# Performance work log

Measured on AMD Instinct MI355X. Metric: run time of the kernel, lower is better.

## Reference

```python
import jax, jax.numpy as jnp
import numpy as np

N_NODES = 10000
N_MOTIFS = 2500          # N_NODES / subgraph_size(=4)
N_AUG = N_NODES + N_MOTIFS
N_EDGES = 500000
NFEAT = 512
NHID = 128


def setup_inputs() -> dict:
    key = jax.random.key(0)
    ks = jax.random.split(key, 14)
    s = 0.05  # param init scale
    return {
        "x": jax.random.normal(ks[0], (N_NODES, NFEAT), jnp.float32),
        "edge_index": jax.random.randint(ks[1], (2, N_EDGES), 0, N_AUG, jnp.int64),
        "motif_list": jax.random.randint(ks[2], (N_MOTIFS, 4), 0, N_NODES, jnp.int64),
        "W1": jax.random.normal(ks[3], (NFEAT, 2 * NHID), jnp.float32) * s,
        "a_src1": jax.random.normal(ks[4], (2 * NHID,), jnp.float32) * s,
        "a_dst1": jax.random.normal(ks[5], (2 * NHID,), jnp.float32) * s,
        "b1": jnp.zeros((2 * NHID,), jnp.float32),
        "W2": jax.random.normal(ks[6], (2 * NHID, NHID), jnp.float32) * s,
        "a_src2": jax.random.normal(ks[7], (NHID,), jnp.float32) * s,
        "a_dst2": jax.random.normal(ks[8], (NHID,), jnp.float32) * s,
        "b2": jnp.zeros((NHID,), jnp.float32),
        "W_lin": jax.random.normal(ks[9], (NFEAT, NHID), jnp.float32) * s,  # torch Linear(nhid, nfeat) weight
        "b_lin": jnp.zeros((NFEAT,), jnp.float32),
    }


def gat_layer(x, src, dst, W, a_s, a_d, b, n):
    """Single-head GATConv (PyG semantics): edge-softmax attention over dst."""
    h = x @ W                                              # [n, out]
    alpha_s = h @ a_s                                      # [n]
    alpha_d = h @ a_d                                      # [n]
    e = jax.nn.leaky_relu(alpha_s[src] + alpha_d[dst], 0.2)  # [E]
    m = jax.ops.segment_max(e, dst, num_segments=n)        # stable softmax per dst
    w = jnp.exp(e - m[dst])
    denom = jax.ops.segment_sum(w, dst, num_segments=n)
    coef = w / (denom[dst] + 1e-16)                        # [E]
    out = jax.ops.segment_sum(coef[:, None] * h[src], dst, num_segments=n)
    return out + b


def reference(x, edge_index, motif_list, W1, a_src1, a_dst1, b1,
              W2, a_src2, a_dst2, b2, W_lin, b_lin):
    n = x.shape[0] + motif_list.shape[0]
    # augmented features: mean of each motif's node features appended as motif nodes
    x_aug = jnp.concatenate([x, jnp.mean(x[motif_list], axis=1)], axis=0)  # [N_AUG, F]
    # augmented edge list + self loops (GATConv adds self loops)
    loops = jnp.arange(n, dtype=edge_index.dtype)
    src = jnp.concatenate([edge_index[0], loops])
    dst = jnp.concatenate([edge_index[1], loops])
    h1 = gat_layer(x_aug, src, dst, W1, a_src1, a_dst1, b1, n)   # [N_AUG, 2*NHID]
    h2 = gat_layer(h1, src, dst, W2, a_src2, a_dst2, b2, n)      # [N_AUG, NHID]
    rec_adj = jax.nn.sigmoid(h2 @ h2.T)                          # [N_AUG, N_AUG]
    rec_feature = jax.nn.sigmoid(h2 @ W_lin.T + b_lin)           # [N_AUG, NFEAT]
    return (rec_feature, rec_adj)
```

## Files before the change

### kernel.cpp

```cpp
#include <hip/hip_runtime.h>

typedef unsigned short u16;
typedef unsigned int   u32;
typedef __attribute__((ext_vector_type(8))) short short8;
typedef __attribute__((ext_vector_type(4))) float f32x4;

#define N_NODES 10000
#define N_MOTIFS 2500
#define N_AUG   12500
#define N_EDGES 500000
#define E_TOT   512500
#define NFEAT   512
#define NH1     256
#define NH2     128

__device__ __forceinline__ float b2f(u16 u){ return __uint_as_float(((u32)u) << 16); }
__device__ __forceinline__ u16 f2b(float f){
  u32 x = __float_as_uint(f);
  x += 0x7fffu + ((x >> 16) & 1u);
  return (u16)(x >> 16);
}

#define PREP_Z   (N_AUG + 8)
#define PREP_W1  (NFEAT * NH1)
#define PREP_W2  (NH1 * NH2)
#define PREP_WL  (NFEAT * NH2)
#define PREP_B   (NH2)
#define PREP_TOT (PREP_Z + PREP_W1 + PREP_W2 + PREP_WL + PREP_B)

__global__ void k_prep(const float* __restrict__ W1, const float* __restrict__ W2,
                       const float* __restrict__ Wl, const float* __restrict__ b1,
                       int* __restrict__ cnt,
                       u16* __restrict__ W1T, u16* __restrict__ W2T, u16* __restrict__ Wlb,
                       float* __restrict__ b1W2){
  int i = blockIdx.x * blockDim.x + threadIdx.x;
  if (i < PREP_Z){ cnt[i] = 0; return; }
  i -= PREP_Z;
  if (i < PREP_W1){
    int r = i / NH1, c = i - r * NH1;
    W1T[(size_t)c * NFEAT + r] = f2b(W1[i]);
    return;
  }
  i -= PREP_W1;
  if (i < PREP_W2){
    int r = i / NH2, c = i - r * NH2;
    W2T[(size_t)c * NH1 + r] = f2b(W2[i]);
    return;
  }
  i -= PREP_W2;
  if (i < PREP_WL){ Wlb[i] = f2b(Wl[i]); return; }
  i -= PREP_WL;
  if (i < PREP_B){
    float s = 0.f;
    #pragma unroll 8
    for (int k = 0; k < NH1; ++k) s += b1[k] * W2[(size_t)k * NH2 + i];
    b1W2[i] = s;
  }
}

__global__ void k_xaug(const float* __restrict__ x, const int* __restrict__ motif,
                       u16* __restrict__ xb){
  int gid = blockIdx.x * blockDim.x + threadIdx.x;
  int row = gid >> 6;
  int c   = (gid & 63) << 3;
  if (row >= N_AUG) return;
  float v[8];
  if (row < N_NODES){
    const float* s = &x[(size_t)row * NFEAT + c];
    #pragma unroll
    for (int k = 0; k < 8; ++k) v[k] = s[k];
  } else {
    int m = row - N_NODES;
    const float* p0 = &x[(size_t)motif[m*4+0] * NFEAT + c];
    const float* p1 = &x[(size_t)motif[m*4+1] * NFEAT + c];
    const float* p2 = &x[(size_t)motif[m*4+2] * NFEAT + c];
    const float* p3 = &x[(size_t)motif[m*4+3] * NFEAT + c];
    #pragma unroll
    for (int k = 0; k < 8; ++k) v[k] = (p0[k] + p1[k] + p2[k] + p3[k]) * 0.25f;
  }
  short8 o;
  #pragma unroll
  for (int k = 0; k < 8; ++k) o[k] = (short)f2b(v[k]);
  *(short8*)&xb[(size_t)row * NFEAT + c] = o;
}

__global__ void k_hist(const int* __restrict__ ei, int* __restrict__ cnt){
  int i = blockIdx.x * blockDim.x + threadIdx.x;
  if (i >= E_TOT) return;
  int d = (i < N_EDGES) ? ei[N_EDGES + i] : (i - N_EDGES);
  atomicAdd(&cnt[d], 1);
}

__global__ void k_scan(const int* __restrict__ cnt, int* __restrict__ offs, int* __restrict__ cur){
  __shared__ int part[1024];
  int t = threadIdx.x;
  const int CH = 13;
  int base = t * CH;
  int s = 0;
  for (int i = 0; i < CH; ++i){ int idx = base + i; if (idx < N_AUG) s += cnt[idx]; }
  part[t] = s;
  __syncthreads();
  for (int off = 1; off < 1024; off <<= 1){
    int v = 0;
    if (t >= off) v = part[t - off];
    __syncthreads();
    if (t >= off) part[t] += v;
    __syncthreads();
  }
  int run = (t == 0) ? 0 : part[t - 1];
  for (int i = 0; i < CH; ++i){
    int idx = base + i;
    if (idx <= N_AUG){
      offs[idx] = run;
      if (idx < N_AUG){ cur[idx] = run; run += cnt[idx]; }
    }
  }
}

__global__ void k_scatter(const int* __restrict__ ei, int* __restrict__ cur, int* __restrict__ srcs){
  int i = blockIdx.x * blockDim.x + threadIdx.x;
  if (i >= E_TOT) return;
  int s, d;
  if (i < N_EDGES){ s = ei[i]; d = ei[N_EDGES + i]; } else { s = i - N_EDGES; d = s; }
  int pos = atomicAdd(&cur[d], 1);
  srcs[pos] = s;
}

template<int DIM>
__global__ void k_alpha(const u16* __restrict__ h, const float* __restrict__ avs,
                        const float* __restrict__ avd, float* __restrict__ oS, float* __restrict__ oD){
  __shared__ float shS[8], shD[8];
  int n = blockIdx.x, t = threadIdx.x;
  int lane = t & 63, wid = t >> 6;
  float hv = b2f(h[(size_t)n * DIM + t]);
  float s = hv * avs[t];
  float d = hv * avd[t];
  #pragma unroll
  for (int o = 32; o; o >>= 1){ s += __shfl_down(s, o); d += __shfl_down(d, o); }
  if (lane == 0){ shS[wid] = s; shD[wid] = d; }
  __syncthreads();
  if (t == 0){
    float ss = 0.f, dd = 0.f;
    #pragma unroll
    for (int i = 0; i < DIM/64; ++i){ ss += shS[i]; dd += shD[i]; }
    oS[n] = ss; oD[n] = dd;
  }
}

__global__ __launch_bounds__(64) void k_agg128(
    const int* __restrict__ offs, const int* __restrict__ srcs,
    const float* __restrict__ aS, const float* __restrict__ aD,
    const u16* __restrict__ hb, const float* __restrict__ bias,
    u16* __restrict__ hout){
  __shared__ float wsh[128];
  __shared__ int   ssh[128];
  int d = blockIdx.x, t = threadIdx.x;
  int r0 = offs[d], r1 = offs[d + 1];
  float adv = aD[d];

  float a0 = 0.f, a1 = 0.f, smp = 0.f;
  for (int base = r0; base < r1; base += 128){
    int cntE = min(128, r1 - base);
    __syncthreads();
    for (int j = t; j < cntE; j += 64){
      int s = srcs[base + j];
      ssh[j] = s;
      float e = aS[s] + adv;
      e = (e >= 0.f) ? e : 0.2f * e;
      float w = __expf(e);
      wsh[j] = w;
      smp += w;
    }
    __syncthreads();
    #pragma unroll 4
    for (int j = 0; j < cntE; ++j){
      u32 v = *(const u32*)&hb[(size_t)ssh[j] * NH2 + 2*t];
      float w = wsh[j];
      a0 = fmaf(w, b2f((u16)(v & 0xffffu)), a0);
      a1 = fmaf(w, b2f((u16)(v >> 16)), a1);
    }
  }
  #pragma unroll
  for (int o = 32; o; o >>= 1) smp += __shfl_down(smp, o);
  smp = __shfl(smp, 0);
  float inv = 1.f / (smp + 1e-16f);
  float o0 = a0 * inv + bias[2*t];
  float o1 = a1 * inv + bias[2*t + 1];
  u32 pv = (u32)f2b(o0) | ((u32)f2b(o1) << 16);
  *(u32*)&hout[(size_t)d * NH2 + 2*t] = pv;
}

template<int EPI>
__global__ __launch_bounds__(256) void k_gemm(
    const u16* __restrict__ A, const u16* __restrict__ B,
    void* __restrict__ Cv, const float* __restrict__ bias,
    int M, int N, int K){
  __shared__ union SM {
    struct { u16 As[128][72]; u16 Bs[128][72]; } ab;
    float stage[64][132];
  } sm;
  int t = threadIdx.x;
  int lane = t & 63, wid = t >> 6;
  int wm = wid >> 1, wn = wid & 1;
  int m0 = blockIdx.y * 128, n0 = blockIdx.x * 128;

  f32x4 acc[4][4];
  #pragma unroll
  for (int i = 0; i < 4; ++i)
    #pragma unroll
    for (int j = 0; j < 4; ++j)
      acc[i][j] = {0.f, 0.f, 0.f, 0.f};

  for (int k0 = 0; k0 < K; k0 += 64){
    __syncthreads();
    #pragma unroll
    for (int i = 0; i < 4; ++i){
      int id = t + i * 256;
      int r = id >> 3, c = (id & 7) << 3;
      int gm = m0 + r; if (gm >= M) gm = M - 1;
      int gn = n0 + r; if (gn >= N) gn = N - 1;
      *(short8*)&sm.ab.As[r][c] = *(const short8*)&A[(size_t)gm * K + k0 + c];
      *(short8*)&sm.ab.Bs[r][c] = *(const short8*)&B[(size_t)gn * K + k0 + c];
    }
    __syncthreads();
    #pragma unroll
    for (int kk = 0; kk < 2; ++kk){
      int kof = kk * 32 + (lane >> 4) * 8;
      short8 af[4], bfr[4];
      #pragma unroll
      for (int mi = 0; mi < 4; ++mi) af[mi]  = *(const short8*)&sm.ab.As[wm*64 + mi*16 + (lane & 15)][kof];
      #pragma unroll
      for (int ni = 0; ni < 4; ++ni) bfr[ni] = *(const short8*)&sm.ab.Bs[wn*64 + ni*16 + (lane & 15)][kof];
      #pragma unroll
      for (int mi = 0; mi < 4; ++mi)
        #pragma unroll
        for (int ni = 0; ni < 4; ++ni)
          acc[mi][ni] = __builtin_amdgcn_mfma_f32_16x16x32_bf16(af[mi], bfr[ni], acc[mi][ni], 0, 0, 0);
    }
  }

  if (EPI == 0){
    u16* C = (u16*)Cv;
    #pragma unroll
    for (int mi = 0; mi < 4; ++mi)
      #pragma unroll
      for (int ni = 0; ni < 4; ++ni){
        int gn = n0 + wn*64 + ni*16 + (lane & 15);
        if (gn >= N) continue;
        #pragma unroll
        for (int r = 0; r < 4; ++r){
          int gm = m0 + wm*64 + mi*16 + (lane >> 4)*4 + r;
          if (gm >= M) continue;
          C[(size_t)gm * N + gn] = f2b(acc[mi][ni][r]);
        }
      }
  } else {
    float* C = (float*)Cv;
    #pragma unroll
    for (int half = 0; half < 2; ++half){
      __syncthreads();
      if (wm == half){
        #pragma unroll
        for (int mi = 0; mi < 4; ++mi)
          #pragma unroll
          for (int ni = 0; ni < 4; ++ni){
            int col = wn*64 + ni*16 + (lane & 15);
            int gn  = n0 + col;
            int gnc = (gn < N) ? gn : (N - 1);
            #pragma unroll
            for (int r = 0; r < 4; ++r){
              int lrow = mi*16 + (lane >> 4)*4 + r;
              float v = acc[mi][ni][r];
              if (EPI == 2) v += bias[gnc];
              v = 1.f / (1.f + __expf(-v));
              sm.stage[lrow][col] = v;
            }
          }
      }
      __syncthreads();
      #pragma unroll
      for (int pss = 0; pss < 8; ++pss){
        int flat = pss * 1024 + t * 4;
        int lr = flat >> 7, c = flat & 127;
        int gm = m0 + half*64 + lr;
        if (gm >= M) continue;
        int gn = n0 + c;
        f32x4 v = *(const f32x4*)&sm.stage[lr][c];
        if (gn + 3 < N){
          __builtin_nontemporal_store(v, (f32x4*)&C[(size_t)gm * N + gn]);
        } else {
          #pragma unroll
          for (int e = 0; e < 4; ++e)
            if (gn + e < N) C[(size_t)gm * N + gn + e] = v[e];
        }
      }
    }
  }
}

extern "C" void kernel_launch(void* const* d_in, const int* in_sizes, int n_in,
                              void* d_out, int out_size, void* d_ws, size_t ws_size,
                              hipStream_t stream){
  const float* x    = (const float*)d_in[0];
  const int*   ei   = (const int*)d_in[1];
  const int*   mot  = (const int*)d_in[2];
  const float* W1   = (const float*)d_in[3];
  const float* a_s1 = (const float*)d_in[4];
  const float* a_d1 = (const float*)d_in[5];
  const float* b1   = (const float*)d_in[6];
  const float* W2   = (const float*)d_in[7];
  const float* a_s2 = (const float*)d_in[8];
  const float* a_d2 = (const float*)d_in[9];
  const float* b2   = (const float*)d_in[10];
  const float* Wl   = (const float*)d_in[11];
  const float* bl   = (const float*)d_in[12];

  char* p = (char*)d_ws;
  auto alloc = [&](size_t bytes){ void* r = (void*)p; p += (bytes + 255) & ~(size_t)255; return r; };
  u16*   xaugb  = (u16*)alloc((size_t)N_AUG * NFEAT * 2);
  u16*   W1T    = (u16*)alloc((size_t)NH1 * NFEAT * 2);
  u16*   W2T    = (u16*)alloc((size_t)NH2 * NH1 * 2);
  u16*   Wlb    = (u16*)alloc((size_t)NFEAT * NH2 * 2);
  u16*   h1b    = (u16*)alloc((size_t)N_AUG * NH1 * 2);
  u16*   g      = (u16*)alloc((size_t)N_AUG * NH2 * 2);
  u16*   h2preb = (u16*)alloc((size_t)N_AUG * NH2 * 2);
  u16*   h2o    = (u16*)alloc((size_t)N_AUG * NH2 * 2);
  float* aS     = (float*)alloc((size_t)N_AUG * 4);
  float* aD     = (float*)alloc((size_t)N_AUG * 4);
  float* b1W2   = (float*)alloc((size_t)NH2 * 4);
  int*   cnt    = (int*)alloc((size_t)(N_AUG + 8) * 4);
  int*   offs   = (int*)alloc((size_t)(N_AUG + 8) * 4);
  int*   cur    = (int*)alloc((size_t)(N_AUG + 8) * 4);
  int*   srcs   = (int*)alloc((size_t)E_TOT * 4);

  float* out_feat = (float*)d_out;
  float* out_adj  = out_feat + (size_t)N_AUG * NFEAT;

  k_prep<<<(PREP_TOT + 255) / 256, 256, 0, stream>>>(W1, W2, Wl, b1, cnt, W1T, W2T, Wlb, b1W2);
  k_xaug<<<(N_AUG * 64 + 255) / 256, 256, 0, stream>>>(x, mot, xaugb);
  k_hist<<<(E_TOT + 255) / 256, 256, 0, stream>>>(ei, cnt);
  k_scan<<<1, 1024, 0, stream>>>(cnt, offs, cur);
  k_scatter<<<(E_TOT + 255) / 256, 256, 0, stream>>>(ei, cur, srcs);

  { dim3 gr(NH1 / 128, 98); k_gemm<0><<<gr, 256, 0, stream>>>(xaugb, W1T, h1b, nullptr, N_AUG, NH1, NFEAT); }
  k_alpha<NH1><<<N_AUG, NH1, 0, stream>>>(h1b, a_s1, a_d1, aS, aD);
  { dim3 gr(1, 98); k_gemm<0><<<gr, 256, 0, stream>>>(h1b, W2T, g, nullptr, N_AUG, NH2, NH1); }
  k_agg128<<<N_AUG, 64, 0, stream>>>(offs, srcs, aS, aD, g, b1W2, h2preb);

  k_alpha<NH2><<<N_AUG, NH2, 0, stream>>>(h2preb, a_s2, a_d2, aS, aD);
  k_agg128<<<N_AUG, 64, 0, stream>>>(offs, srcs, aS, aD, h2preb, b2, h2o);

  { dim3 gr(NFEAT / 128, 98); k_gemm<2><<<gr, 256, 0, stream>>>(h2o, Wlb, out_feat, bl, N_AUG, NFEAT, NH2); }
  { dim3 gr(98, 98);          k_gemm<1><<<gr, 256, 0, stream>>>(h2o, h2o, out_adj, nullptr, N_AUG, N_AUG, NH2); }
}
```

Baseline: 432.2 us.

## Replace adjacency GEMM with row-strip kernel sweeping all column tiles

Adds a dedicated k_adj kernel for sigmoid(h2 h2^T). Each block keeps a 16-row strip of h2 in shared memory and loops over all 98 column tiles, reloading each 128-row B tile and writing 16x128 sigmoid outputs. Output stores change from nontemporal to regular stores, and the generic epilogue now always adds bias. This targets the write-dominated 625MB output with a different blocking, but each block re-reads all of h2 and syncs three times per tile, and the 782-block grid with small 16-row tiles may reduce MFMA efficiency.

New measurement: 547.8 us. 26.8% more time.

```diff
diff --git a/kernel.cpp b/kernel.cpp
--- a/kernel.cpp
+++ b/kernel.cpp
@@ -190,6 +190,76 @@
   *(u32*)&hout[(size_t)d * NH2 + 2*t] = pv;
 }
 
+__global__ __launch_bounds__(256) void k_adj(const u16* __restrict__ H,
+                                             float* __restrict__ C){
+  __shared__ u16   Asm[16][136];
+  __shared__ u16   Bsm[128][132];
+  __shared__ float Cst[16][132];
+  int t = threadIdx.x;
+  int lane = t & 63, w = t >> 6;
+  int r0 = blockIdx.x * 16;
+
+  {
+    int flat = t * 8;
+    int r = flat >> 7, c = flat & 127;
+    int gr = r0 + r; if (gr >= N_AUG) gr = N_AUG - 1;
+    *(short8*)&Asm[r][c] = *(const short8*)&H[(size_t)gr * NH2 + c];
+  }
+
+  for (int j = 0; j < 98; ++j){
+    int n0 = j * 128;
+    #pragma unroll
+    for (int q = 0; q < 8; ++q){
+      int flat = q * 2048 + t * 8;
+      int r = flat >> 7, c = flat & 127;
+      int gr = n0 + r; if (gr >= N_AUG) gr = N_AUG - 1;
+      *(short8*)&Bsm[r][c] = *(const short8*)&H[(size_t)gr * NH2 + c];
+    }
+    __syncthreads();
+
+    f32x4 acc0 = {0.f,0.f,0.f,0.f}, acc1 = {0.f,0.f,0.f,0.f};
+    #pragma unroll
+    for (int ks = 0; ks < 4; ++ks){
+      int kof = ks * 32 + (lane >> 4) * 8;
+      short8 a  = *(const short8*)&Asm[lane & 15][kof];
+      short8 b0 = *(const short8*)&Bsm[w*32 + (lane & 15)][kof];
+      short8 b1 = *(const short8*)&Bsm[w*32 + 16 + (lane & 15)][kof];
+      acc0 = __builtin_amdgcn_mfma_f32_16x16x32_bf16(a, b0, acc0, 0, 0, 0);
+      acc1 = __builtin_amdgcn_mfma_f32_16x16x32_bf16(a, b1, acc1, 0, 0, 0);
+    }
+    __syncthreads();
+
+    #pragma unroll
+    for (int ni = 0; ni < 2; ++ni){
+      int col = w*32 + ni*16 + (lane & 15);
+      const f32x4& av = ni ? acc1 : acc0;
+      #pragma unroll
+      for (int r = 0; r < 4; ++r){
+        float v = av[r];
+        Cst[(lane >> 4)*4 + r][col] = 1.f / (1.f + __expf(-v));
+      }
+    }
+    __syncthreads();
+
+    #pragma unroll
+    for (int pss = 0; pss < 2; ++pss){
+      int flat = pss * 1024 + t * 4;
+      int rl = flat >> 7, c = flat & 127;
+      int gm = r0 + rl;
+      if (gm >= N_AUG) continue;
+      int gn = n0 + c;
+      f32x4 v = *(const f32x4*)&Cst[rl][c];
+      if (gn + 3 < N_AUG){
+        *(f32x4*)&C[(size_t)gm * N_AUG + gn] = v;
+      } else {
+        #pragma unroll
+        for (int e = 0; e < 4; ++e)
+          if (gn + e < N_AUG) C[(size_t)gm * N_AUG + gn + e] = v[e];
+      }
+    }
+  }
+}
+
 template<int EPI>
 __global__ __launch_bounds__(256) void k_gemm(
     const u16* __restrict__ A, const u16* __restrict__ B,
@@ -271,7 +341,7 @@
             for (int r = 0; r < 4; ++r){
               int lrow = mi*16 + (lane >> 4)*4 + r;
               float v = acc[mi][ni][r];
-              if (EPI == 2) v += bias[gnc];
+              v += bias[gnc];
               v = 1.f / (1.f + __expf(-v));
               sm.stage[lrow][col] = v;
             }
@@ -287,7 +357,7 @@
         int gn = n0 + c;
         f32x4 v = *(const f32x4*)&sm.stage[lr][c];
         if (gn + 3 < N){
-          __builtin_nontemporal_store(v, (f32x4*)&C[(size_t)gm * N + gn]);
+          *(f32x4*)&C[(size_t)gm * N + gn] = v;
         } else {
           #pragma unroll
           for (int e = 0; e < 4; ++e)
@@ -351,5 +421,5 @@
   k_agg128<<<N_AUG, 64, 0, stream>>>(offs, srcs, aS, aD, h2preb, b2, h2o);
 
   { dim3 gr(NFEAT / 128, 98); k_gemm<2><<<gr, 256, 0, stream>>>(h2o, Wlb, out_feat, bl, N_AUG, NFEAT, NH2); }
-  { dim3 gr(98, 98);          k_gemm<1><<<gr, 256, 0, stream>>>(h2o, h2o, out_adj, nullptr, N_AUG, N_AUG, NH2); }
-}
+  k_adj<<<(N_AUG + 15) / 16, 256, 0, stream>>>(h2o, out_adj);
+}
```
